# Kernel optimization log

Hardware: AMD Instinct MI355X
Metric: run time of the kernel (lower is better)

The kernel has to match this reference:

```python
import jax, jax.numpy as jnp
import numpy as np

B, C, H, W = 4, 256, 128, 256
NUM_CODES = 256  # codebook rows; dim_code == C


def setup_inputs() -> dict:
    key = jax.random.key(0)
    k_feat, k_code = jax.random.split(key)
    feature = jax.random.normal(k_feat, (B, C, H, W), dtype=jnp.float32)
    codebook = jax.random.normal(k_code, (NUM_CODES, C), dtype=jnp.float32)
    return {"feature": feature, "codebook": codebook}


def reference(feature, codebook):
    # Faithful to ComminPub.sender core:
    #   weights = (feature_expand * codebooks).sum(dim=2) / (codebooks*codebooks).sum(dim=2)
    # expressed as a contraction over C instead of materializing [B,N,C,H,W].
    code_norm = jnp.sum(codebook * codebook, axis=1)          # [N]
    weights = jnp.einsum('bchw,nc->bnhw', feature, codebook)   # [B,N,H,W]
    weights = weights / code_norm[None, :, None, None]
    # fc_after_rbdc reconstruction: einsum('b n h w, n c -> b c h w', weights, codebook)
    recon = jnp.einsum('bnhw,nc->bchw', weights, codebook)     # [B,C,H,W]
    return recon
```

## Files before the change

### kernel.cpp

```cpp
#include <hip/hip_runtime.h>
#include <hip/hip_bf16.h>
#include <cstdint>

#define CDIM   256
#define NCODES 256
#define HWB    32768
#define BATCH  4
#define BN     128
#define TPB    512
#define LROW   36

typedef __bf16  bf16x8 __attribute__((ext_vector_type(8)));
typedef __bf16  bf16x2 __attribute__((ext_vector_type(2)));
typedef float   f32x4  __attribute__((ext_vector_type(4)));
typedef float   f32x2  __attribute__((ext_vector_type(2)));
typedef uint32_t u32x2 __attribute__((ext_vector_type(2)));
typedef uint32_t u32x4 __attribute__((ext_vector_type(4)));

__global__ __launch_bounds__(256) void prep_kernel(const float* __restrict__ cb,
                                                   __bf16* __restrict__ Mpk) {
    __shared__ f32x2 s2[NCODES];
    const int i0 = blockIdx.x * 2;
    const int j  = threadIdx.x;

    const float* row = cb + (size_t)j * CDIM;
    float nrm = 0.f;
#pragma unroll 8
    for (int c = 0; c < CDIM; c += 4) {
        f32x4 v = *(const f32x4*)(row + c);
        nrm += v[0] * v[0] + v[1] * v[1] + v[2] * v[2] + v[3] * v[3];
    }
    const float inv = 1.0f / nrm;
    s2[j] = (f32x2){row[i0] * inv, row[i0 + 1] * inv};
    __syncthreads();

    f32x2 acc = {0.f, 0.f};
#pragma unroll 16
    for (int n = 0; n < NCODES; ++n) {
        const float cv = cb[(size_t)n * CDIM + j];
        const f32x2 sv = s2[n];
        acc[0] += sv[0] * cv;
        acc[1] += sv[1] * cv;
    }
    const int base = ((j >> 3) * 256) * 8 + (j & 7);
    Mpk[base + (size_t)(i0    ) * 8] = (__bf16)acc[0];
    Mpk[base + (size_t)(i0 + 1) * 8] = (__bf16)acc[1];
}

__global__ __launch_bounds__(TPB, 2) void recon_kernel(
    const float* __restrict__ feat, const __bf16* __restrict__ Mpk,
    float* __restrict__ out) {
    __shared__ __align__(16) __bf16 Blds[2][BN * LROW];

    const int tid  = threadIdx.x;
    const int lane = tid & 63;
    const int w    = tid >> 6;
    const int quad = lane >> 4;
    const int l16  = lane & 15;
    const int c0   = w * 32;

    bf16x8 mreg[2][8];
#pragma unroll
    for (int ct = 0; ct < 2; ++ct)
#pragma unroll
        for (int kc = 0; kc < 8; ++kc)
            mreg[ct][kc] = *(const bf16x8*)(
                Mpk + (size_t)((kc * 4 + quad) * 256 + c0 + ct * 16 + l16) * 8);

    const int b  = blockIdx.x >> 8;
    const int p0 = (blockIdx.x & 255) * BN;

    const int px4 = tid & 31;
    const int kp  = tid >> 5;
    const float* f0 = feat + (size_t)b * CDIM * HWB + p0 + px4 * 4;

    f32x4 acc[8][2];
#pragma unroll
    for (int mt = 0; mt < 8; ++mt)
#pragma unroll
        for (int ct = 0; ct < 2; ++ct)
            acc[mt][ct] = (f32x4){0.f, 0.f, 0.f, 0.f};

    f32x4 fva[2], fvb[2];
#pragma unroll
    for (int s = 0; s < 2; ++s) {
        fva[s] = *(const f32x4*)(f0 + (size_t)(s * 32 + 2 * kp) * HWB);
        fvb[s] = *(const f32x4*)(f0 + (size_t)(s * 32 + 2 * kp + 1) * HWB);
    }

    const int rbase = l16 * 18 + quad * 4;

#pragma unroll
    for (int i = 0; i < 8; ++i) {
        const int sl = i & 1;
        __bf16* wb = &Blds[i & 1][0] + (px4 * 4) * LROW + 2 * kp;
#pragma unroll
        for (int e = 0; e < 4; ++e) {
            bf16x2 p;
            p[0] = (__bf16)fva[sl][e];
            p[1] = (__bf16)fvb[sl][e];
            *(bf16x2*)(wb + (size_t)e * LROW) = p;
        }
        if (i < 6) {
            fva[sl] = *(const f32x4*)(f0 + (size_t)((i + 2) * 32 + 2 * kp) * HWB);
            fvb[sl] = *(const f32x4*)(f0 + (size_t)((i + 2) * 32 + 2 * kp + 1) * HWB);
        }
        asm volatile("s_waitcnt lgkmcnt(0)\n\ts_barrier" ::: "memory");
        const uint32_t* lr = (const uint32_t*)(&Blds[i & 1][0]);
#pragma unroll
        for (int mt = 0; mt < 8; ++mt) {
            u32x2 lo = *(const u32x2*)(lr + rbase + mt * 288);
            u32x2 hi = *(const u32x2*)(lr + rbase + mt * 288 + 2);
            bf16x8 af = __builtin_bit_cast(bf16x8, (u32x4){lo[0], lo[1], hi[0], hi[1]});
            acc[mt][0] = __builtin_amdgcn_mfma_f32_16x16x32_bf16(
                af, mreg[0][i], acc[mt][0], 0, 0, 0);
            acc[mt][1] = __builtin_amdgcn_mfma_f32_16x16x32_bf16(
                af, mreg[1][i], acc[mt][1], 0, 0, 0);
        }
    }

    float* ob = out + (size_t)b * CDIM * HWB + p0 + quad * 4;
#pragma unroll
    for (int mt = 0; mt < 8; ++mt)
#pragma unroll
        for (int ct = 0; ct < 2; ++ct)
            *(f32x4*)(ob + (size_t)(c0 + ct * 16 + l16) * HWB + mt * 16) =
                acc[mt][ct];
}

extern "C" void kernel_launch(void* const* d_in, const int* in_sizes, int n_in,
                              void* d_out, int out_size, void* d_ws, size_t ws_size,
                              hipStream_t stream) {
    const float* feat = (const float*)d_in[0];
    const float* cb   = (const float*)d_in[1];
    float* out = (float*)d_out;

    __bf16* Mpk = (__bf16*)d_ws;

    prep_kernel<<<NCODES / 2, 256, 0, stream>>>(cb, Mpk);

    const int nblocks = BATCH * (HWB / BN);
    recon_kernel<<<nblocks, TPB, 0, stream>>>(feat, Mpk, out);
}
```

Measured before the change: 248.4 us.

## Double pixel tile per block, restructure feature loads and vectorize LDS reads

Each block now processes 256 pixels instead of 128, halving the grid and amortizing the per-block codebook register preload. Each thread loads 4 channels of 4 pixels with nontemporal loads and writes packed bf16x4 to LDS, so MFMA operands are read as single 16-byte LDS loads. The larger accumulator array raises register pressure, which risks spills or lower occupancy.

```diff
diff --git a/kernel.cpp b/kernel.cpp
--- a/kernel.cpp
+++ b/kernel.cpp
@@ -6,16 +6,14 @@
 #define NCODES 256
 #define HWB    32768
 #define BATCH  4
-#define BN     128
+#define BN     256
 #define TPB    512
 #define LROW   36
 
 typedef __bf16  bf16x8 __attribute__((ext_vector_type(8)));
-typedef __bf16  bf16x2 __attribute__((ext_vector_type(2)));
+typedef __bf16  bf16x4 __attribute__((ext_vector_type(4)));
 typedef float   f32x4  __attribute__((ext_vector_type(4)));
 typedef float   f32x2  __attribute__((ext_vector_type(2)));
-typedef uint32_t u32x2 __attribute__((ext_vector_type(2)));
-typedef uint32_t u32x4 __attribute__((ext_vector_type(4)));
 
 __global__ __launch_bounds__(256) void prep_kernel(const float* __restrict__ cb,
                                                    __bf16* __restrict__ Mpk) {
@@ -67,51 +65,51 @@
             mreg[ct][kc] = *(const bf16x8*)(
                 Mpk + (size_t)((kc * 4 + quad) * 256 + c0 + ct * 16 + l16) * 8);
 
-    const int b  = blockIdx.x >> 8;
-    const int p0 = (blockIdx.x & 255) * BN;
+    const int b  = blockIdx.x >> 7;
+    const int p0 = (blockIdx.x & 127) * BN;
 
-    const int px4 = tid & 31;
-    const int kp  = tid >> 5;
+    const int px4 = tid & 63;
+    const int kq  = tid >> 6;
     const float* f0 = feat + (size_t)b * CDIM * HWB + p0 + px4 * 4;
 
-    f32x4 acc[8][2];
+    f32x4 acc[16][2];
 #pragma unroll
-    for (int mt = 0; mt < 8; ++mt)
+    for (int mt = 0; mt < 16; ++mt)
 #pragma unroll
         for (int ct = 0; ct < 2; ++ct)
             acc[mt][ct] = (f32x4){0.f, 0.f, 0.f, 0.f};
 
-    f32x4 fva[2], fvb[2];
+    f32x4 L[2][4];
 #pragma unroll
-    for (int s = 0; s < 2; ++s) {
-        fva[s] = *(const f32x4*)(f0 + (size_t)(s * 32 + 2 * kp) * HWB);
-        fvb[s] = *(const f32x4*)(f0 + (size_t)(s * 32 + 2 * kp + 1) * HWB);
-    }
-
-    const int rbase = l16 * 18 + quad * 4;
+    for (int r = 0; r < 4; ++r)
+        L[0][r] = __builtin_nontemporal_load(
+            (const f32x4*)(f0 + (size_t)(4 * kq + r) * HWB));
 
 #pragma unroll
     for (int i = 0; i < 8; ++i) {
         const int sl = i & 1;
-        __bf16* wb = &Blds[i & 1][0] + (px4 * 4) * LROW + 2 * kp;
+        if (i < 7) {
+            const float* fn = f0 + (size_t)((i + 1) * 32 + 4 * kq) * HWB;
+#pragma unroll
+            for (int r = 0; r < 4; ++r)
+                L[sl ^ 1][r] = __builtin_nontemporal_load(
+                    (const f32x4*)(fn + (size_t)r * HWB));
+        }
+        __bf16* wb = &Blds[sl][0] + (px4 * 4) * LROW + 4 * kq;
 #pragma unroll
         for (int e = 0; e < 4; ++e) {
-            bf16x2 p;
-            p[0] = (__bf16)fva[sl][e];
-            p[1] = (__bf16)fvb[sl][e];
-            *(bf16x2*)(wb + (size_t)e * LROW) = p;
-        }
-        if (i < 6) {
-            fva[sl] = *(const f32x4*)(f0 + (size_t)((i + 2) * 32 + 2 * kp) * HWB);
-            fvb[sl] = *(const f32x4*)(f0 + (size_t)((i + 2) * 32 + 2 * kp + 1) * HWB);
+            bf16x4 p;
+            p[0] = (__bf16)L[sl][0][e];
+            p[1] = (__bf16)L[sl][1][e];
+            p[2] = (__bf16)L[sl][2][e];
+            p[3] = (__bf16)L[sl][3][e];
+            *(bf16x4*)(wb + (size_t)e * LROW) = p;
         }
         asm volatile("s_waitcnt lgkmcnt(0)\n\ts_barrier" ::: "memory");
-        const uint32_t* lr = (const uint32_t*)(&Blds[i & 1][0]);
 #pragma unroll
-        for (int mt = 0; mt < 8; ++mt) {
-            u32x2 lo = *(const u32x2*)(lr + rbase + mt * 288);
-            u32x2 hi = *(const u32x2*)(lr + rbase + mt * 288 + 2);
-            bf16x8 af = __builtin_bit_cast(bf16x8, (u32x4){lo[0], lo[1], hi[0], hi[1]});
+        for (int mt = 0; mt < 16; ++mt) {
+            bf16x8 af = *(const bf16x8*)(
+                &Blds[sl][0] + (mt * 16 + l16) * LROW + quad * 8);
             acc[mt][0] = __builtin_amdgcn_mfma_f32_16x16x32_bf16(
                 af, mreg[0][i], acc[mt][0], 0, 0, 0);
             acc[mt][1] = __builtin_amdgcn_mfma_f32_16x16x32_bf16(
@@ -121,7 +119,7 @@
 
     float* ob = out + (size_t)b * CDIM * HWB + p0 + quad * 4;
 #pragma unroll
-    for (int mt = 0; mt < 8; ++mt)
+    for (int mt = 0; mt < 16; ++mt)
 #pragma unroll
         for (int ct = 0; ct < 2; ++ct)
             *(f32x4*)(ob + (size_t)(c0 + ct * 16 + l16) * HWB + mt * 16) =
```

New measurement: 240.4 us. 1.03x faster.
